# Performance work log

Hardware: AMD Instinct MI355X
Metric: run time of the kernel (lower is better)

Reference implementation:

```python
import jax, jax.numpy as jnp
import numpy as np

B, NX, NY, NZ = 2, 64, 64, 64
D, CI, CO, F = 3, 32, 32, 64  # spatial dims, chan in/out, n_modes


def setup_inputs() -> dict:
    key = jax.random.key(0)
    ka, kx, ky, k1, k2, k3, k4, k5, k6 = jax.random.split(key, 9)
    omega, c = 30.0 / 300.0, 6.0
    u = lambda k, shape, scale: scale * (2.0 * jax.random.uniform(k, shape, jnp.float32) - 1.0)
    return {
        "a": jax.random.normal(ka, (B, NX, NY, NZ, CI), jnp.float32),
        "x": jax.random.uniform(kx, (B, NX, NY, NZ, D), jnp.float32),
        "y": jax.random.uniform(ky, (B, NX, NY, NZ, D), jnp.float32),
        "modes_a": u(k1, (F, CI), np.sqrt(c / (CI + F))),
        "modes_x": u(k2, (F, D), np.sqrt(c / (D + F)) * omega),
        "modes_y": u(k3, (F, D), np.sqrt(c / (D + F)) * omega),
        "modes_u": u(k4, (F, CO), np.sqrt(c / (F + CO))),
        "fc_w": jax.random.normal(k5, (CI, CO), jnp.float32) / np.sqrt(CI),
        "fc_b": jax.random.normal(k6, (CO,), jnp.float32) * 0.01,
    }


def reference(a, x, y, modes_a, modes_x, modes_y, modes_u, fc_w, fc_b):
    # SpectralAttention: Fourier-feature linear attention.
    # NOTE: source forward passes x for both coordinate args (att(h, x, x)).
    A = jnp.einsum('bxyzi,fi->bxyzf', a, modes_a)                       # [B,NX,NY,NZ,F]
    X = jnp.exp(-2j * np.pi * jnp.einsum('bxyzd,gd->bxyzg', x, modes_x))  # complex64
    Y = jnp.exp(2j * np.pi * jnp.einsum('bxyzd,gd->bxyzg', x, modes_y))   # complex64
    N = x.shape[1] * x.shape[2] * x.shape[3]
    AX = jnp.einsum('bxyzf,bxyzg->bfg', A.astype(X.dtype), X)           # [B,F,F] complex
    U = jnp.einsum('bfg,bxyzg->bxyzf', AX, Y).real / N                  # [B,NX,NY,NZ,F]
    u = jnp.einsum('bxyzf,fo->bxyzo', U, modes_u)                        # [B,NX,NY,NZ,CO]
    h = u + a @ fc_w + fc_b                                              # residual Linear
    return jax.nn.gelu(h)
```

## Files before the change

### kernel.cpp

```cpp
#include <hip/hip_runtime.h>
#include <math.h>

#define NB   2
#define NPTS 262144

typedef __attribute__((ext_vector_type(8))) __bf16 bf16x8;
typedef __attribute__((ext_vector_type(4))) float  f32x4;

__device__ __forceinline__ float gelu_fast(float v) {
    float t  = v * v;
    float z2 = v * (-2.302208f + -0.1029432f * t);
    float e  = __builtin_amdgcn_exp2f(z2);
    return v * __builtin_amdgcn_rcpf(1.0f + e);
}

__device__ __forceinline__ unsigned short bf16_rn(float f) {
    unsigned u = __builtin_bit_cast(unsigned, f);
    u += 0x7fffu + ((u >> 16) & 1u);
    return (unsigned short)(u >> 16);
}

__global__ __launch_bounds__(256)
void pass1_kernel(const float* __restrict__ a, const float* __restrict__ x,
                  const float* __restrict__ mx, float* __restrict__ part, int NPB)
{
    __shared__ float4 xs[4][32];
    __shared__ float wsum[32 * 129];

    const int t = threadIdx.x, wave = t >> 6, lane = t & 63;
    const int l15 = lane & 15, l4 = lane >> 4;
    const int blk = blockIdx.x, b = blk / NPB, pb = blk % NPB;
    const int ppb = NPTS / NPB;
    const int chunks = ppb >> 5;
    const long base = (long)b * NPTS + (long)pb * ppb;

    float m0[4], m1[4], m2[4];
    #pragma unroll
    for (int ct = 0; ct < 4; ++ct) {
        int g = l15 + 16 * ct;
        m0[ct] = mx[g*3]; m1[ct] = mx[g*3+1]; m2[ct] = mx[g*3+2];
    }

    f32x4 acc[2][8];
    #pragma unroll
    for (int rt = 0; rt < 2; ++rt)
        #pragma unroll
        for (int ct = 0; ct < 8; ++ct)
            acc[rt][ct] = f32x4{0.f, 0.f, 0.f, 0.f};

    for (int ci = wave; ci < chunks; ci += 4) {
        const long p0 = base + ((long)ci << 5);
        if (lane < 32) {
            const float* xq = x + (p0 + lane) * 3;
            xs[wave][lane] = make_float4(xq[0], xq[1], xq[2], 0.f);
        }
        bf16x8 afr[2];
        #pragma unroll
        for (int j = 0; j < 8; ++j) {
            float2 av = *(const float2*)(a + (p0 + l4*8 + j) * 32 + 2*l15);
            afr[0][j] = (__bf16)av.x;
            afr[1][j] = (__bf16)av.y;
        }

        float4 xp[8];
        #pragma unroll
        for (int j = 0; j < 8; ++j) xp[j] = xs[wave][l4*8 + j];

        #pragma unroll
        for (int ct = 0; ct < 4; ++ct) {
            bf16x8 bc, bs;
            #pragma unroll
            for (int j = 0; j < 8; ++j) {
                float d = xp[j].x*m0[ct] + xp[j].y*m1[ct] + xp[j].z*m2[ct];
                bc[j] = (__bf16)__builtin_amdgcn_cosf(d);
                bs[j] = (__bf16)__builtin_amdgcn_sinf(d);
            }
            #pragma unroll
            for (int rt = 0; rt < 2; ++rt) {
                acc[rt][ct]   = __builtin_amdgcn_mfma_f32_16x16x32_bf16(afr[rt], bc, acc[rt][ct],   0, 0, 0);
                acc[rt][ct+4] = __builtin_amdgcn_mfma_f32_16x16x32_bf16(afr[rt], bs, acc[rt][ct+4], 0, 0, 0);
            }
        }
    }

    for (int w = 0; w < 4; ++w) {
        if (wave == w) {
            #pragma unroll
            for (int rt = 0; rt < 2; ++rt)
                #pragma unroll
                for (int ct = 0; ct < 8; ++ct)
                    #pragma unroll
                    for (int r = 0; r < 4; ++r) {
                        int i = 2 * (l4*4 + r) + rt;
                        int c = ((ct & 3) * 16) + l15 + ((ct & 4) ? 64 : 0);
                        int id = i * 129 + c;
                        float v = acc[rt][ct][r];
                        if (w == 0) wsum[id] = v; else wsum[id] += v;
                    }
        }
        __syncthreads();
    }
    for (int idx = t; idx < 4096; idx += 256) {
        int i = idx >> 7, c = idx & 127;
        part[(long)blk * 4096 + idx] = wsum[i * 129 + c];
    }
}

__global__ __launch_bounds__(256)
void reduceW_kernel(const float* __restrict__ part, float* __restrict__ Wf, int NPB)
{
    __shared__ float red[8][33];
    const int t = threadIdx.x;
    const int b = blockIdx.x >> 7;
    const int jb = (blockIdx.x & 127) * 32;
    const int jj = jb + (t & 31), seg = t >> 5;
    const float* p = part + (long)b * NPB * 4096 + jj;
    float s = 0.f;
    for (int pb = seg; pb < NPB; pb += 8) s += p[(long)pb * 4096];
    red[seg][t & 31] = s;
    __syncthreads();
    if (t < 32) {
        float r = 0.f;
        #pragma unroll
        for (int q = 0; q < 8; ++q) r += red[q][t];
        Wf[b * 4096 + jb + t] = r;
    }
}

__global__ __launch_bounds__(256)
void vmat_kernel(const float* __restrict__ Wf, const float* __restrict__ ma,
                 const float* __restrict__ mu, const float* __restrict__ fcw,
                 unsigned short* __restrict__ Vb)
{
    __shared__ float Ws[4096];
    __shared__ float Mas[64 * 32], Mus[64 * 32];
    __shared__ float Qs[32][32];
    const int t = threadIdx.x, b = blockIdx.x;

    for (int i = t; i < 4096; i += 256) Ws[i] = Wf[b * 4096 + i];
    for (int i = t; i < 2048; i += 256) { Mas[i] = ma[i]; Mus[i] = mu[i]; }
    __syncthreads();
    for (int i = t; i < 1024; i += 256) {
        int o = i >> 5, ii = i & 31;
        float s = 0.f;
        for (int f = 0; f < 64; ++f) s += Mus[f*32 + o] * Mas[f*32 + ii];
        Qs[o][ii] = s;
    }
    __syncthreads();
    const float invN = 1.f / 262144.f;
    for (int i = t; i < 5120; i += 256) {
        int k = i >> 5, o = i & 31;
        float v;
        if (k < 128) {
            int g = k & 63, off = (k >= 64) ? 64 : 0;
            float s = 0.f;
            for (int q = 0; q < 32; ++q) s += Qs[o][q] * Ws[q*128 + off + g];
            v = s * invN;
        } else {
            v = fcw[(k - 128) * 32 + o];
        }
        Vb[b * 5120 + i] = bf16_rn(v);
    }
}

__global__ __launch_bounds__(256)
void pass2_kernel(const float* __restrict__ a, const float* __restrict__ x,
                  const unsigned short* __restrict__ Vb, const float* __restrict__ fcb,
                  const float* __restrict__ my, float* __restrict__ out)
{
    __shared__ float4 xs[4][32];
    __shared__ float4 mys[64];
    const int t = threadIdx.x, wave = t >> 6, lane = t & 63;
    const int l15 = lane & 15, l4 = lane >> 4;
    const int blk = blockIdx.x, b = blk >> 9, lb = blk & 511;
    const long base = (long)b * NPTS + (long)lb * 512;

    if (t < 64) { const float* mq = my + t*3; mys[t] = make_float4(mq[0], mq[1], mq[2], 0.f); }

    bf16x8 bfr[5][2];
    {
        const unsigned short* vb = Vb + b * 5120;
        #pragma unroll
        for (int c = 0; c < 5; ++c)
            #pragma unroll
            for (int ct = 0; ct < 2; ++ct) {
                bf16x8 tmp;
                #pragma unroll
                for (int j = 0; j < 8; ++j) {
                    unsigned short uv = vb[(32*c + l4*8 + j) * 32 + l15 + 16*ct];
                    tmp[j] = __builtin_bit_cast(__bf16, uv);
                }
                bfr[c][ct] = tmp;
            }
    }
    const float bias0 = fcb[l15], bias1 = fcb[l15 + 16];
    __syncthreads();

    for (int ci = wave; ci < 16; ci += 4) {
        const long p0 = base + ((long)ci << 5);
        if (lane < 32) {
            const float* xq = x + (p0 + lane) * 3;
            xs[wave][lane] = make_float4(xq[0], xq[1], xq[2], 0.f);
        }
        bf16x8 afr[2];
        #pragma unroll
        for (int rt = 0; rt < 2; ++rt) {
            const float* ap = a + (p0 + l15 + 16*rt) * 32 + l4*8;
            float4 a0 = *(const float4*)ap;
            float4 a1 = *(const float4*)(ap + 4);
            afr[rt][0] = (__bf16)a0.x; afr[rt][1] = (__bf16)a0.y;
            afr[rt][2] = (__bf16)a0.z; afr[rt][3] = (__bf16)a0.w;
            afr[rt][4] = (__bf16)a1.x; afr[rt][5] = (__bf16)a1.y;
            afr[rt][6] = (__bf16)a1.z; afr[rt][7] = (__bf16)a1.w;
        }
        float4 xp0 = xs[wave][l15];
        float4 xp1 = xs[wave][l15 + 16];

        f32x4 acc[2][2];
        #pragma unroll
        for (int rt = 0; rt < 2; ++rt)
            #pragma unroll
            for (int ct = 0; ct < 2; ++ct)
                acc[rt][ct] = f32x4{0.f, 0.f, 0.f, 0.f};

        #pragma unroll
        for (int gt = 0; gt < 2; ++gt) {
            bf16x8 ac[2], as2[2];
            #pragma unroll
            for (int j = 0; j < 8; ++j) {
                float4 m = mys[gt*32 + l4*8 + j];
                float d0 = xp0.x*m.x + xp0.y*m.y + xp0.z*m.z;
                float d1 = xp1.x*m.x + xp1.y*m.y + xp1.z*m.z;
                ac[0][j]  = (__bf16)__builtin_amdgcn_cosf(d0);
                as2[0][j] = (__bf16)__builtin_amdgcn_sinf(d0);
                ac[1][j]  = (__bf16)__builtin_amdgcn_cosf(d1);
                as2[1][j] = (__bf16)__builtin_amdgcn_sinf(d1);
            }
            #pragma unroll
            for (int rt = 0; rt < 2; ++rt)
                #pragma unroll
                for (int ct = 0; ct < 2; ++ct) {
                    acc[rt][ct] = __builtin_amdgcn_mfma_f32_16x16x32_bf16(ac[rt],  bfr[gt][ct],   acc[rt][ct], 0, 0, 0);
                    acc[rt][ct] = __builtin_amdgcn_mfma_f32_16x16x32_bf16(as2[rt], bfr[2+gt][ct], acc[rt][ct], 0, 0, 0);
                }
        }
        #pragma unroll
        for (int rt = 0; rt < 2; ++rt)
            #pragma unroll
            for (int ct = 0; ct < 2; ++ct) {
                acc[rt][ct] = __builtin_amdgcn_mfma_f32_16x16x32_bf16(afr[rt], bfr[4][ct], acc[rt][ct], 0, 0, 0);
                float bias = ct ? bias1 : bias0;
                #pragma unroll
                for (int r = 0; r < 4; ++r) {
                    long p = p0 + 16*rt + l4*4 + r;
                    out[p * 32 + l15 + 16*ct] = gelu_fast(acc[rt][ct][r] + bias);
                }
            }
    }
}

extern "C" void kernel_launch(void* const* d_in, const int* in_sizes, int n_in,
                              void* d_out, int out_size, void* d_ws, size_t ws_size,
                              hipStream_t stream)
{
    const float* a   = (const float*)d_in[0];
    const float* x   = (const float*)d_in[1];
    const float* ma  = (const float*)d_in[3];
    const float* mx  = (const float*)d_in[4];
    const float* my  = (const float*)d_in[5];
    const float* mu  = (const float*)d_in[6];
    const float* fcw = (const float*)d_in[7];
    const float* fcb = (const float*)d_in[8];
    float* out = (float*)d_out;

    int NPB = 512;
    while (NPB > 32) {
        size_t need = (size_t)NB * NPB * 4096 * 4 + (size_t)NB * 4096 * 4
                    + (size_t)NB * 5120 * 2 + 256;
        if (need <= ws_size) break;
        NPB >>= 1;
    }
    float* part = (float*)d_ws;
    float* Wf = part + (size_t)NB * NPB * 4096;
    unsigned short* Vb = (unsigned short*)(Wf + NB * 4096);

    pass1_kernel<<<NB * NPB, 256, 0, stream>>>(a, x, mx, part, NPB);
    reduceW_kernel<<<NB * 128, 256, 0, stream>>>(part, Wf, NPB);
    vmat_kernel<<<NB, 256, 0, stream>>>(Wf, ma, mu, fcw, Vb);
    pass2_kernel<<<NB * 512, 256, 0, stream>>>(a, x, Vb, fcb, my, out);
}
```

Measured before the change: 90.83 us.

## Register-prefetch next chunk's a/x in pass1 and pass2, halve pass1 blocks

```diff
diff --git a/kernel.cpp b/kernel.cpp
--- a/kernel.cpp
+++ b/kernel.cpp
@@ -48,23 +48,46 @@
         for (int ct = 0; ct < 8; ++ct)
             acc[rt][ct] = f32x4{0.f, 0.f, 0.f, 0.f};
 
-    for (int ci = wave; ci < chunks; ci += 4) {
-        const long p0 = base + ((long)ci << 5);
+    {
+        const long p0 = base + ((long)wave << 5);
         if (lane < 32) {
             const float* xq = x + (p0 + lane) * 3;
             xs[wave][lane] = make_float4(xq[0], xq[1], xq[2], 0.f);
         }
+    }
+    float2 aq[8];
+    {
+        const long p0 = base + ((long)wave << 5);
+        #pragma unroll
+        for (int j = 0; j < 8; ++j)
+            aq[j] = *(const float2*)(a + (p0 + l4*8 + j) * 32 + 2*l15);
+    }
+
+    for (int ci = wave; ci < chunks; ci += 4) {
+        const bool hasnext = (ci + 4) < chunks;
+        const long pn = base + ((long)(ci + 4) << 5);
+
         bf16x8 afr[2];
         #pragma unroll
         for (int j = 0; j < 8; ++j) {
-            float2 av = *(const float2*)(a + (p0 + l4*8 + j) * 32 + 2*l15);
-            afr[0][j] = (__bf16)av.x;
-            afr[1][j] = (__bf16)av.y;
+            afr[0][j] = (__bf16)aq[j].x;
+            afr[1][j] = (__bf16)aq[j].y;
         }
 
         float4 xp[8];
         #pragma unroll
         for (int j = 0; j < 8; ++j) xp[j] = xs[wave][l4*8 + j];
+
+        float2 anq[8];
+        if (hasnext) {
+            #pragma unroll
+            for (int j = 0; j < 8; ++j)
+                anq[j] = *(const float2*)(a + (pn + l4*8 + j) * 32 + 2*l15);
+            if (lane < 32) {
+                const float* xq = x + (pn + lane) * 3;
+                xs[wave][lane] = make_float4(xq[0], xq[1], xq[2], 0.f);
+            }
+        }
 
         #pragma unroll
         for (int ct = 0; ct < 4; ++ct) {
@@ -80,6 +103,11 @@
                 acc[rt][ct]   = __builtin_amdgcn_mfma_f32_16x16x32_bf16(afr[rt], bc, acc[rt][ct],   0, 0, 0);
                 acc[rt][ct+4] = __builtin_amdgcn_mfma_f32_16x16x32_bf16(afr[rt], bs, acc[rt][ct+4], 0, 0, 0);
             }
+        }
+
+        if (hasnext) {
+            #pragma unroll
+            for (int j = 0; j < 8; ++j) aq[j] = anq[j];
         }
     }
 
@@ -133,17 +161,14 @@
                  unsigned short* __restrict__ Vb)
 {
     __shared__ float Ws[4096];
-    __shared__ float Mas[64 * 32], Mus[64 * 32];
     __shared__ float Qs[32][32];
     const int t = threadIdx.x, b = blockIdx.x;
-
     for (int i = t; i < 4096; i += 256) Ws[i] = Wf[b * 4096 + i];
-    for (int i = t; i < 2048; i += 256) { Mas[i] = ma[i]; Mus[i] = mu[i]; }
     __syncthreads();
     for (int i = t; i < 1024; i += 256) {
         int o = i >> 5, ii = i & 31;
         float s = 0.f;
-        for (int f = 0; f < 64; ++f) s += Mus[f*32 + o] * Mas[f*32 + ii];
+        for (int f = 0; f < 64; ++f) s += mu[f*32 + o] * ma[f*32 + ii];
         Qs[o][ii] = s;
     }
     __syncthreads();
@@ -196,13 +221,16 @@
     const float bias0 = fcb[l15], bias1 = fcb[l15 + 16];
     __syncthreads();
 
-    for (int ci = wave; ci < 16; ci += 4) {
-        const long p0 = base + ((long)ci << 5);
+    {
+        const long p0 = base + ((long)wave << 5);
         if (lane < 32) {
             const float* xq = x + (p0 + lane) * 3;
             xs[wave][lane] = make_float4(xq[0], xq[1], xq[2], 0.f);
         }
-        bf16x8 afr[2];
+    }
+    bf16x8 afr[2];
+    {
+        const long p0 = base + ((long)wave << 5);
         #pragma unroll
         for (int rt = 0; rt < 2; ++rt) {
             const float* ap = a + (p0 + l15 + 16*rt) * 32 + l4*8;
@@ -213,15 +241,39 @@
             afr[rt][4] = (__bf16)a1.x; afr[rt][5] = (__bf16)a1.y;
             afr[rt][6] = (__bf16)a1.z; afr[rt][7] = (__bf16)a1.w;
         }
+    }
+
+    for (int ci = wave; ci < 16; ci += 4) {
+        const long pc = base + ((long)ci << 5);
+        const bool hasnext = (ci + 4) < 16;
+        const long pn = base + ((long)(ci + 4) << 5);
+
         float4 xp0 = xs[wave][l15];
         float4 xp1 = xs[wave][l15 + 16];
 
+        bf16x8 anfr[2];
+        if (hasnext) {
+            #pragma unroll
+            for (int rt = 0; rt < 2; ++rt) {
+                const float* ap = a + (pn + l15 + 16*rt) * 32 + l4*8;
+                float4 a0 = *(const float4*)ap;
+                float4 a1 = *(const float4*)(ap + 4);
+                anfr[rt][0] = (__bf16)a0.x; anfr[rt][1] = (__bf16)a0.y;
+                anfr[rt][2] = (__bf16)a0.z; anfr[rt][3] = (__bf16)a0.w;
+                anfr[rt][4] = (__bf16)a1.x; anfr[rt][5] = (__bf16)a1.y;
+                anfr[rt][6] = (__bf16)a1.z; anfr[rt][7] = (__bf16)a1.w;
+            }
+            if (lane < 32) {
+                const float* xq = x + (pn + lane) * 3;
+                xs[wave][lane] = make_float4(xq[0], xq[1], xq[2], 0.f);
+            }
+        }
+
         f32x4 acc[2][2];
         #pragma unroll
         for (int rt = 0; rt < 2; ++rt)
             #pragma unroll
-            for (int ct = 0; ct < 2; ++ct)
-                acc[rt][ct] = f32x4{0.f, 0.f, 0.f, 0.f};
+            for (int ct = 0; ct < 2; ++ct) acc[rt][ct] = f32x4{0.f,0.f,0.f,0.f};
 
         #pragma unroll
         for (int gt = 0; gt < 2; ++gt) {
@@ -252,10 +304,12 @@
                 float bias = ct ? bias1 : bias0;
                 #pragma unroll
                 for (int r = 0; r < 4; ++r) {
-                    long p = p0 + 16*rt + l4*4 + r;
+                    long p = pc + 16*rt + l4*4 + r;
                     out[p * 32 + l15 + 16*ct] = gelu_fast(acc[rt][ct][r] + bias);
                 }
             }
+
+        if (hasnext) { afr[0] = anfr[0]; afr[1] = anfr[1]; }
     }
 }
 
@@ -273,10 +327,9 @@
     const float* fcb = (const float*)d_in[8];
     float* out = (float*)d_out;
 
-    int NPB = 512;
+    int NPB = 256;
     while (NPB > 32) {
-        size_t need = (size_t)NB * NPB * 4096 * 4 + (size_t)NB * 4096 * 4
-                    + (size_t)NB * 5120 * 2 + 256;
+        size_t need = ((size_t)NB * NPB * 4096 + 16384) * sizeof(float);
         if (need <= ws_size) break;
         NPB >>= 1;
     }
```

Measured after the change: 86.70 us. 1.05x faster.

## Cache bf16 copy of activations in pass1 and store partials as bf16

Applied to the files above, without the earlier changes.

```diff
diff --git a/kernel.cpp b/kernel.cpp
--- a/kernel.cpp
+++ b/kernel.cpp
@@ -20,9 +20,15 @@
     return (unsigned short)(u >> 16);
 }
 
+__device__ __forceinline__ float bf16_to_f32(unsigned short h) {
+    return __builtin_bit_cast(float, (unsigned)h << 16);
+}
+
+template<bool WRITE_ABF>
 __global__ __launch_bounds__(256)
 void pass1_kernel(const float* __restrict__ a, const float* __restrict__ x,
-                  const float* __restrict__ mx, float* __restrict__ part, int NPB)
+                  const float* __restrict__ mx, unsigned short* __restrict__ part16,
+                  unsigned* __restrict__ abf, int NPB)
 {
     __shared__ float4 xs[4][32];
     __shared__ float wsum[32 * 129];
@@ -49,17 +55,23 @@
             acc[rt][ct] = f32x4{0.f, 0.f, 0.f, 0.f};
 
     for (int ci = wave; ci < chunks; ci += 4) {
-        const long p0 = base + ((long)ci << 5);
+        const long pc = base + ((long)ci << 5);
+
         if (lane < 32) {
-            const float* xq = x + (p0 + lane) * 3;
+            const float* xq = x + (pc + lane) * 3;
             xs[wave][lane] = make_float4(xq[0], xq[1], xq[2], 0.f);
         }
+
         bf16x8 afr[2];
         #pragma unroll
         for (int j = 0; j < 8; ++j) {
-            float2 av = *(const float2*)(a + (p0 + l4*8 + j) * 32 + 2*l15);
-            afr[0][j] = (__bf16)av.x;
-            afr[1][j] = (__bf16)av.y;
+            float2 av = *(const float2*)(a + (pc + l4*8 + j) * 32 + 2*l15);
+            unsigned short h0 = bf16_rn(av.x);
+            unsigned short h1 = bf16_rn(av.y);
+            if (WRITE_ABF)
+                abf[(pc + l4*8 + j) * 16 + l15] = (unsigned)h0 | ((unsigned)h1 << 16);
+            afr[0][j] = __builtin_bit_cast(__bf16, h0);
+            afr[1][j] = __builtin_bit_cast(__bf16, h1);
         }
 
         float4 xp[8];
@@ -102,21 +114,22 @@
     }
     for (int idx = t; idx < 4096; idx += 256) {
         int i = idx >> 7, c = idx & 127;
-        part[(long)blk * 4096 + idx] = wsum[i * 129 + c];
+        part16[(long)blk * 4096 + idx] = bf16_rn(wsum[i * 129 + c]);
     }
 }
 
 __global__ __launch_bounds__(256)
-void reduceW_kernel(const float* __restrict__ part, float* __restrict__ Wf, int NPB)
+void reduceW_kernel(const unsigned short* __restrict__ part16,
+                    float* __restrict__ Wf, int NPB)
 {
     __shared__ float red[8][33];
     const int t = threadIdx.x;
     const int b = blockIdx.x >> 7;
     const int jb = (blockIdx.x & 127) * 32;
     const int jj = jb + (t & 31), seg = t >> 5;
-    const float* p = part + (long)b * NPB * 4096 + jj;
+    const unsigned short* p = part16 + (long)b * NPB * 4096 + jj;
     float s = 0.f;
-    for (int pb = seg; pb < NPB; pb += 8) s += p[(long)pb * 4096];
+    for (int pb = seg; pb < NPB; pb += 8) s += bf16_to_f32(p[(long)pb * 4096]);
     red[seg][t & 31] = s;
     __syncthreads();
     if (t < 32) {
@@ -133,17 +146,14 @@
                  unsigned short* __restrict__ Vb)
 {
     __shared__ float Ws[4096];
-    __shared__ float Mas[64 * 32], Mus[64 * 32];
     __shared__ float Qs[32][32];
     const int t = threadIdx.x, b = blockIdx.x;
-
     for (int i = t; i < 4096; i += 256) Ws[i] = Wf[b * 4096 + i];
-    for (int i = t; i < 2048; i += 256) { Mas[i] = ma[i]; Mus[i] = mu[i]; }
     __syncthreads();
     for (int i = t; i < 1024; i += 256) {
         int o = i >> 5, ii = i & 31;
         float s = 0.f;
-        for (int f = 0; f < 64; ++f) s += Mus[f*32 + o] * Mas[f*32 + ii];
+        for (int f = 0; f < 64; ++f) s += mu[f*32 + o] * ma[f*32 + ii];
         Qs[o][ii] = s;
     }
     __syncthreads();
@@ -163,10 +173,12 @@
     }
 }
 
+template<bool READ_ABF>
 __global__ __launch_bounds__(256)
-void pass2_kernel(const float* __restrict__ a, const float* __restrict__ x,
-                  const unsigned short* __restrict__ Vb, const float* __restrict__ fcb,
-                  const float* __restrict__ my, float* __restrict__ out)
+void pass2_kernel(const float* __restrict__ a, const unsigned* __restrict__ abf,
+                  const float* __restrict__ x, const unsigned short* __restrict__ Vb,
+                  const float* __restrict__ fcb, const float* __restrict__ my,
+                  float* __restrict__ out)
 {
     __shared__ float4 xs[4][32];
     __shared__ float4 mys[64];
@@ -197,22 +209,30 @@
     __syncthreads();
 
     for (int ci = wave; ci < 16; ci += 4) {
-        const long p0 = base + ((long)ci << 5);
+        const long pc = base + ((long)ci << 5);
+
         if (lane < 32) {
-            const float* xq = x + (p0 + lane) * 3;
+            const float* xq = x + (pc + lane) * 3;
             xs[wave][lane] = make_float4(xq[0], xq[1], xq[2], 0.f);
         }
+
         bf16x8 afr[2];
         #pragma unroll
         for (int rt = 0; rt < 2; ++rt) {
-            const float* ap = a + (p0 + l15 + 16*rt) * 32 + l4*8;
-            float4 a0 = *(const float4*)ap;
-            float4 a1 = *(const float4*)(ap + 4);
-            afr[rt][0] = (__bf16)a0.x; afr[rt][1] = (__bf16)a0.y;
-            afr[rt][2] = (__bf16)a0.z; afr[rt][3] = (__bf16)a0.w;
-            afr[rt][4] = (__bf16)a1.x; afr[rt][5] = (__bf16)a1.y;
-            afr[rt][6] = (__bf16)a1.z; afr[rt][7] = (__bf16)a1.w;
-        }
+            if (READ_ABF) {
+                afr[rt] = __builtin_bit_cast(bf16x8,
+                    *(const uint4*)(abf + (pc + l15 + 16*rt) * 16 + l4*4));
+            } else {
+                const float* ap = a + (pc + l15 + 16*rt) * 32 + l4*8;
+                float4 a0 = *(const float4*)ap;
+                float4 a1 = *(const float4*)(ap + 4);
+                afr[rt][0] = (__bf16)a0.x; afr[rt][1] = (__bf16)a0.y;
+                afr[rt][2] = (__bf16)a0.z; afr[rt][3] = (__bf16)a0.w;
+                afr[rt][4] = (__bf16)a1.x; afr[rt][5] = (__bf16)a1.y;
+                afr[rt][6] = (__bf16)a1.z; afr[rt][7] = (__bf16)a1.w;
+            }
+        }
+
         float4 xp0 = xs[wave][l15];
         float4 xp1 = xs[wave][l15 + 16];
 
@@ -220,8 +240,7 @@
         #pragma unroll
         for (int rt = 0; rt < 2; ++rt)
             #pragma unroll
-            for (int ct = 0; ct < 2; ++ct)
-                acc[rt][ct] = f32x4{0.f, 0.f, 0.f, 0.f};
+            for (int ct = 0; ct < 2; ++ct) acc[rt][ct] = f32x4{0.f,0.f,0.f,0.f};
 
         #pragma unroll
         for (int gt = 0; gt < 2; ++gt) {
@@ -252,7 +271,7 @@
                 float bias = ct ? bias1 : bias0;
                 #pragma unroll
                 for (int r = 0; r < 4; ++r) {
-                    long p = p0 + 16*rt + l4*4 + r;
+                    long p = pc + 16*rt + l4*4 + r;
                     out[p * 32 + l15 + 16*ct] = gelu_fast(acc[rt][ct][r] + bias);
                 }
             }
@@ -273,19 +292,33 @@
     const float* fcb = (const float*)d_in[8];
     float* out = (float*)d_out;
 
+    const size_t abfB = (size_t)NB * NPTS * 16 * 4;
+    const size_t WfB  = (size_t)NB * 4096 * 4;
+    const size_t VbB  = (size_t)NB * 5120 * 2;
+
     int NPB = 512;
-    while (NPB > 32) {
-        size_t need = (size_t)NB * NPB * 4096 * 4 + (size_t)NB * 4096 * 4
-                    + (size_t)NB * 5120 * 2 + 256;
-        if (need <= ws_size) break;
+    bool use_abf = true;
+    while (NPB > 32 &&
+           ws_size < abfB + WfB + (size_t)NB * NPB * 4096 * 2 + VbB + 256)
         NPB >>= 1;
-    }
-    float* part = (float*)d_ws;
-    float* Wf = part + (size_t)NB * NPB * 4096;
-    unsigned short* Vb = (unsigned short*)(Wf + NB * 4096);
-
-    pass1_kernel<<<NB * NPB, 256, 0, stream>>>(a, x, mx, part, NPB);
-    reduceW_kernel<<<NB * 128, 256, 0, stream>>>(part, Wf, NPB);
+    if (ws_size < abfB + WfB + (size_t)NB * NPB * 4096 * 2 + VbB + 256)
+        use_abf = false;
+
+    unsigned* abf = (unsigned*)d_ws;
+    float* Wf = (float*)(abf + (size_t)NB * NPTS * 16);
+    unsigned short* part16 = (unsigned short*)(Wf + NB * 4096);
+    unsigned short* Vb = part16 + (size_t)NB * NPB * 4096;
+
+    if (use_abf)
+        pass1_kernel<true><<<NB * NPB, 256, 0, stream>>>(a, x, mx, part16, abf, NPB);
+    else
+        pass1_kernel<false><<<NB * NPB, 256, 0, stream>>>(a, x, mx, part16, abf, NPB);
+
+    reduceW_kernel<<<NB * 128, 256, 0, stream>>>(part16, Wf, NPB);
     vmat_kernel<<<NB, 256, 0, stream>>>(Wf, ma, mu, fcw, Vb);
-    pass2_kernel<<<NB * 512, 256, 0, stream>>>(a, x, Vb, fcb, my, out);
-}
+
+    if (use_abf)
+        pass2_kernel<true><<<NB * 512, 256, 0, stream>>>(a, abf, x, Vb, fcb, my, out);
+    else
+        pass2_kernel<false><<<NB * 512, 256, 0, stream>>>(a, abf, x, Vb, fcb, my, out);
+}
```

Result: no change. 91.82 us (+1.1%).
